# Kernel optimization log

Measured on AMD Instinct MI355X. Metric: run time of the kernel, lower is better.

## Reference

```python
import jax, jax.numpy as jnp
import numpy as np

MAX_SCALE_CAP = 200
STEP = 3


def _shift(a, dy, dx):
    # a[..., y+dy, x+dx] with zero fill outside (dy, dx >= 0), matching the
    # zero-padded dilated 3x3 convs whose only off-center tap is at (+dy,+dx).
    H, W = a.shape[-2], a.shape[-1]
    p = jnp.pad(a, ((0, 0), (0, 0), (0, dy), (0, dx)))
    return p[..., dy:dy + H, dx:dx + W]


def _dif_stacks(Pred, GT, ROI):
    # Builds difPrd / difGT: channel order is (scale major, layer l, direction)
    # directions in dict order: Horizontal (0,+s), Vertical (+s,0), Diagonal (+s,+s)
    B, _, H, W = Pred.shape
    max_scale = min(MAX_SCALE_CAP, max(H, W))
    dP, dG = [], []
    for scale in range(1, max_scale, STEP):
        bP, bG = [], []
        for dy, dx in ((0, scale), (scale, 0), (scale, scale)):
            roi = ROI * _shift(ROI, dy, dx)             # [B,1,H,W]
            bP.append(roi * (Pred - _shift(Pred, dy, dx)))  # [B,3,H,W]
            bG.append(roi * (GT - _shift(GT, dy, dx)))
        # stack dirs on a new axis after layer axis -> l-major, dir-minor
        dP.append(jnp.stack(bP, axis=2).reshape(B, 9, H, W))
        dG.append(jnp.stack(bG, axis=2).reshape(B, 9, H, W))
    return jnp.concatenate(dP, axis=1), jnp.concatenate(dG, axis=1)


def _loss(PredXYZ, GTXYZ, ROIMask):
    difPrd, difGT = _dif_stacks(PredXYZ, GTXYZ, ROIMask)

    # normalization constant per image (detached in the original)
    Rat = jax.nn.relu(difPrd / (difGT + 1e-5))
    absG = jnp.abs(difGT)
    NormConst = (absG * Rat).sum((1, 2, 3)) / ((absG * (Rat > 0)).sum((1, 2, 3)) + 1e-4)
    NormConst = jax.lax.stop_gradient(NormConst)

    c = NormConst                                   # [B]
    safe_c = jnp.where(c > 1e-4, c, 1.0)
    term1 = jnp.where(
        c > 1e-4,
        jnp.abs(difGT - difPrd / safe_c[:, None, None, None]).mean((1, 2, 3)),
        0.0,
    )

    roi_sum = ROIMask.sum((1, 2, 3))
    pos_cnt = (difGT > 0).sum((1, 2, 3)).astype(jnp.float32)
    mean_prd = jnp.abs(difPrd).sum((1, 2, 3)) / pos_cnt

    big = roi_sum > 200
    term2 = jnp.where(big & (mean_prd > 30) & (c > 10), mean_prd - 30.0, 0.0)
    fact = 0.1 / (c + 0.001)
    term3 = jnp.where(big & (mean_prd < 2) & (c < 0.1), (0.2 - mean_prd) * fact, 0.0)

    return (term1 + term2 + term3).sum(), NormConst


def setup_inputs() -> dict:
    key = jax.random.key(0)
    k1, k2, k3 = jax.random.split(key, 3)
    PredXYZ = jax.random.normal(k1, (2, 3, 256, 256), dtype=jnp.float32)
    GTXYZ = jax.random.normal(k2, (2, 3, 256, 256), dtype=jnp.float32)
    ROIMask = (jax.random.uniform(k3, (2, 1, 256, 256)) > 0.3).astype(jnp.float32)
    return {"PredXYZ": PredXYZ, "GTXYZ": GTXYZ, "ROIMask": ROIMask}


def reference(PredXYZ, GTXYZ, ROIMask):
    return _loss(PredXYZ, GTXYZ, ROIMask)
```

## Files before the change

kernel.cpp:

```cpp
#include <hip/hip_runtime.h>


#define NSCALES 67
#define IMG_H 256
#define IMG_W 256
#define NPIX 65536
#define NLINES 2046
#define LMAX_PAD 320


__device__ __forceinline__ double wave_red(double v) {
#pragma unroll
  for (int o = 32; o > 0; o >>= 1) v += __shfl_down(v, o, 64);
  return v;
}

__device__ __forceinline__ void decode_line(int id, int& b, int& base, int& stride, int& L) {
  if (id < 512) {
    b = id >> 8; int y = id & 255;
    base = y * IMG_W; stride = 1; L = IMG_W;
  } else if (id < 1024) {
    int t = id - 512; b = t >> 8;
    base = t & 255; stride = IMG_W; L = IMG_H;
  } else {
    int t = id - 1024; b = (t >= 511) ? 1 : 0;
    int d = t - b * 511; int c = d - 255;
    int ac = (c < 0) ? -c : c;
    base = (c < 0) ? (-c) * IMG_W : c;
    stride = IMG_W + 1; L = 256 - ac;
  }
}

__device__ __forceinline__ int scale_count(int L, int q) {
  int rem = L - 1 - (q << 6);
  int kcnt = (rem >= 1) ? ((rem - 1) / 3 + 1) : 0;
  return (kcnt > NSCALES) ? NSCALES : kcnt;
}

__device__ __forceinline__ float stage_line(
    const float* __restrict__ Pred, const float* __restrict__ GT,
    const float* __restrict__ ROI, int b, int base, int stride, int L,
    int tid, float4* bufA, float4* bufB) {
  const float* P = Pred + b * (3 * NPIX);
  const float* G = GT + b * (3 * NPIX);
  const float* R = ROI + b * NPIX;
  float r = 0.f, p0 = 0.f, p1 = 0.f, p2 = 0.f, g0 = 0.f, g1 = 0.f, g2 = 0.f;
  if (tid < L) {
    int a = base + tid * stride;
    r = R[a];
    p0 = P[a]; p1 = P[a + NPIX]; p2 = P[a + 2 * NPIX];
    g0 = G[a]; g1 = G[a + NPIX]; g2 = G[a + 2 * NPIX];
  }
  bufA[tid] = make_float4(r, p0, p1, p2);
  bufB[tid] = make_float4(g0, g1, g2, 0.f);
  if (tid < LMAX_PAD - 256) {
    bufA[256 + tid] = make_float4(0.f, 0.f, 0.f, 0.f);
    bufB[256 + tid] = make_float4(0.f, 0.f, 0.f, 0.f);
  }
  __syncthreads();
  return r;
}

extern "C" __global__ void __launch_bounds__(256, 8) pass1_kernel(
    const float* __restrict__ Pred, const float* __restrict__ GT,
    const float* __restrict__ ROI, double* __restrict__ ws) {
  __shared__ float4 bufA[LMAX_PAD];
  __shared__ float4 bufB[LMAX_PAD];
  __shared__ double red[4][5];
  const int id = blockIdx.x;
  const int tid = threadIdx.x;
  const int wid = tid >> 6, lane = tid & 63;

  int b, base, stride, L;
  decode_line(id, b, base, stride, L);
  float stg_r = stage_line(Pred, GT, ROI, b, base, stride, L, tid, bufA, bufB);

  float f1 = 0.f, f2 = 0.f, fp = 0.f;
  int pci = 0;
  int P = 0;
  for (int q = 0; q < 4; ++q) {
    const int Kq = scale_count(L, q);
    int k = (wid - P) & 3;
    if (k < Kq) {
      const int c = (q << 6) + lane;
      const float4 cA = bufA[c];
      const float4 cB = bufB[c];
      const float cr = cA.x, cp0 = cA.y, cp1 = cA.z, cp2 = cA.w;
      const float cg0 = cB.x, cg1 = cB.y, cg2 = cB.z;
      const float4* tA = &bufA[c + 1 + 3 * k];
      const float4* tB = &bufB[c + 1 + 3 * k];
#pragma unroll 2
      for (; k < Kq; k += 4) {
        float4 t0 = tA[0];
        float4 t1 = tB[0];
        tA += 12; tB += 12;
        float rr = cr * t0.x;
#define L1BODY(cp, cg, tp, tg)                                   \
        {                                                        \
          float dP = rr * (cp - tp);                             \
          float dG = rr * (cg - tg);                             \
          float qq = dP * __builtin_amdgcn_rcpf(dG + 1e-5f);     \
          float aG = fabsf(dG);                                  \
          f1 += fmaxf(aG * qq, 0.f);                             \
          if (qq > 0.f) f2 += aG;                                \
          if (dG > 0.f) pci++;                                   \
          fp += fabsf(dP);                                       \
        }
        L1BODY(cp0, cg0, t0.y, t1.x)
        L1BODY(cp1, cg1, t0.z, t1.y)
        L1BODY(cp2, cg2, t0.w, t1.z)
#undef L1BODY
      }
    }
    P += Kq;
  }

  double w0 = wave_red((double)f1);
  double w1 = wave_red((double)f2);
  double w2 = wave_red((double)pci);
  double w3 = wave_red((double)fp);
  double w4 = wave_red((double)stg_r);
  if (lane == 0) {
    red[wid][0] = w0; red[wid][1] = w1; red[wid][2] = w2;
    red[wid][3] = w3; red[wid][4] = w4;
  }
  __syncthreads();
  if (tid < 4)
    unsafeAtomicAdd(&ws[b * 4 + tid],
                    red[0][tid] + red[1][tid] + red[2][tid] + red[3][tid]);
  if (tid == 4 && id < 512)
    unsafeAtomicAdd(&ws[8 + b], red[0][4] + red[1][4] + red[2][4] + red[3][4]);
}

extern "C" __global__ void __launch_bounds__(256, 8) pass2_kernel(
    const float* __restrict__ Pred, const float* __restrict__ GT,
    const float* __restrict__ ROI, double* __restrict__ ws) {
  __shared__ float4 bufA[LMAX_PAD];
  __shared__ float4 bufB[LMAX_PAD];
  __shared__ double red[4];
  __shared__ float s_invC;
  const int id = blockIdx.x;
  const int tid = threadIdx.x;
  const int wid = tid >> 6, lane = tid & 63;

  int b, base, stride, L;
  decode_line(id, b, base, stride, L);
  if (tid == 0) {
    double S1 = ws[b * 4 + 0], S2 = ws[b * 4 + 1];
    float cc = (float)(S1 / (S2 + 1e-4));
    s_invC = (cc > 1e-4f) ? (float)(1.0 / (double)cc) : 1.0f;
  }
  stage_line(Pred, GT, ROI, b, base, stride, L, tid, bufA, bufB);

  const float invC = s_invC;
  float f = 0.f;
  int P = 0;
  for (int q = 0; q < 4; ++q) {
    const int Kq = scale_count(L, q);
    int k = (wid - P) & 3;
    if (k < Kq) {
      const int c = (q << 6) + lane;
      const float4 cA = bufA[c];
      const float4 cB = bufB[c];
      const float cr = cA.x, cp0 = cA.y, cp1 = cA.z, cp2 = cA.w;
      const float cg0 = cB.x, cg1 = cB.y, cg2 = cB.z;
      const float4* tA = &bufA[c + 1 + 3 * k];
      const float4* tB = &bufB[c + 1 + 3 * k];
#pragma unroll 2
      for (; k < Kq; k += 4) {
        float4 t0 = tA[0];
        float4 t1 = tB[0];
        tA += 12; tB += 12;
        float rr = cr * t0.x;
        f += rr * fabsf((cg0 - t1.x) - (cp0 - t0.y) * invC);
        f += rr * fabsf((cg1 - t1.y) - (cp1 - t0.z) * invC);
        f += rr * fabsf((cg2 - t1.z) - (cp2 - t0.w) * invC);
      }
    }
    P += Kq;
  }
  double t = wave_red((double)f);
  if (lane == 0) red[wid] = t;
  __syncthreads();
  if (tid == 0)
    unsafeAtomicAdd(&ws[24 + b], red[0] + red[1] + red[2] + red[3]);
}

extern "C" __global__ void __launch_bounds__(64) final_kernel(
    const double* __restrict__ ws, float* __restrict__ out) {
  if (threadIdx.x == 0) {
    double loss = 0.0;
    for (int b = 0; b < 2; ++b) {
      double S1 = ws[b * 4 + 0], S2 = ws[b * 4 + 1];
      double PC = ws[b * 4 + 2], SP = ws[b * 4 + 3];
      double RS = ws[8 + b];
      float cc = (float)(S1 / (S2 + 1e-4));
      out[1 + b] = cc;
      double term1 = (cc > 1e-4f) ? ws[24 + b] / (603.0 * 65536.0) : 0.0;
      float meanPrd = (float)(SP / PC);
      bool big = RS > 200.0;
      float t2 = (big && meanPrd > 30.f && cc > 10.f) ? (meanPrd - 30.f) : 0.f;
      float fact = 0.1f / (cc + 0.001f);
      float t3 = (big && meanPrd < 2.f && cc < 0.1f) ? (0.2f - meanPrd) * fact : 0.f;
      loss += term1 + (double)(t2 + t3);
    }
    out[0] = (float)loss;
  }
}

extern "C" void kernel_launch(void* const* d_in, const int* in_sizes, int n_in,
                              void* d_out, int out_size, void* d_ws, size_t ws_size,
                              hipStream_t stream) {
  (void)in_sizes; (void)n_in; (void)out_size; (void)ws_size;
  const float* Pred = (const float*)d_in[0];
  const float* GT = (const float*)d_in[1];
  const float* ROI = (const float*)d_in[2];
  float* out = (float*)d_out;
  double* ws = (double*)d_ws;

  hipMemsetAsync(d_ws, 0, 32 * sizeof(double), stream);
  hipLaunchKernelGGL(pass1_kernel, dim3(NLINES), dim3(256), 0, stream,
                     Pred, GT, ROI, ws);
  hipLaunchKernelGGL(pass2_kernel, dim3(NLINES), dim3(256), 0, stream,
                     Pred, GT, ROI, ws);
  hipLaunchKernelGGL(final_kernel, dim3(1), dim3(64), 0, stream, ws, out);
}
```

Measured before the change: 128.1 us.

## Replace global atomics with per-block partial slots and drop workspace memset

```diff
diff --git a/kernel.cpp b/kernel.cpp
--- a/kernel.cpp
+++ b/kernel.cpp
@@ -8,6 +8,8 @@
 #define NLINES 2046
 #define LMAX_PAD 320
 
+
+#define SLOT2_BASE 32768
 
 __device__ __forceinline__ double wave_red(double v) {
 #pragma unroll
@@ -125,11 +127,15 @@
     red[wid][3] = w3; red[wid][4] = w4;
   }
   __syncthreads();
-  if (tid < 4)
-    unsafeAtomicAdd(&ws[b * 4 + tid],
-                    red[0][tid] + red[1][tid] + red[2][tid] + red[3][tid]);
-  if (tid == 4 && id < 512)
-    unsafeAtomicAdd(&ws[8 + b], red[0][4] + red[1][4] + red[2][4] + red[3][4]);
+  if (tid < 16) {
+    const int q = tid & 7, tb = tid >> 3;
+    double v = 0.0;
+    if (tb == b && q < 5) {
+      v = red[0][q] + red[1][q] + red[2][q] + red[3][q];
+      if (q == 4 && id >= 512) v = 0.0;
+    }
+    ws[(size_t)id * 16 + tid] = v;
+  }
 }
 
 extern "C" __global__ void __launch_bounds__(256, 8) pass2_kernel(
@@ -138,21 +144,34 @@
   __shared__ float4 bufA[LMAX_PAD];
   __shared__ float4 bufB[LMAX_PAD];
   __shared__ double red[4];
-  __shared__ float s_invC;
+  __shared__ double pre[4][4];
+  __shared__ float s_invC[2];
   const int id = blockIdx.x;
   const int tid = threadIdx.x;
   const int wid = tid >> 6, lane = tid & 63;
 
   int b, base, stride, L;
   decode_line(id, b, base, stride, L);
-  if (tid == 0) {
-    double S1 = ws[b * 4 + 0], S2 = ws[b * 4 + 1];
+
+  double a0 = 0.0, a1 = 0.0, a2 = 0.0, a3 = 0.0;
+  for (int j = tid; j < NLINES; j += 256) {
+    const double* s = ws + (size_t)j * 16;
+    a0 += s[0]; a1 += s[1]; a2 += s[8]; a3 += s[9];
+  }
+  a0 = wave_red(a0); a1 = wave_red(a1); a2 = wave_red(a2); a3 = wave_red(a3);
+  if (lane == 0) {
+    pre[wid][0] = a0; pre[wid][1] = a1; pre[wid][2] = a2; pre[wid][3] = a3;
+  }
+  __syncthreads();
+  if (tid < 2) {
+    double S1 = pre[0][2 * tid] + pre[1][2 * tid] + pre[2][2 * tid] + pre[3][2 * tid];
+    double S2 = pre[0][2 * tid + 1] + pre[1][2 * tid + 1] + pre[2][2 * tid + 1] + pre[3][2 * tid + 1];
     float cc = (float)(S1 / (S2 + 1e-4));
-    s_invC = (cc > 1e-4f) ? (float)(1.0 / (double)cc) : 1.0f;
+    s_invC[tid] = (cc > 1e-4f) ? (float)(1.0 / (double)cc) : 1.0f;
   }
   stage_line(Pred, GT, ROI, b, base, stride, L, tid, bufA, bufB);
 
-  const float invC = s_invC;
+  const float invC = s_invC[b];
   float f = 0.f;
   int P = 0;
   for (int q = 0; q < 4; ++q) {
@@ -182,21 +201,46 @@
   double t = wave_red((double)f);
   if (lane == 0) red[wid] = t;
   __syncthreads();
-  if (tid == 0)
-    unsafeAtomicAdd(&ws[24 + b], red[0] + red[1] + red[2] + red[3]);
-}
-
-extern "C" __global__ void __launch_bounds__(64) final_kernel(
+  if (tid < 2) {
+    double v = (tid == b) ? (red[0] + red[1] + red[2] + red[3]) : 0.0;
+    ws[SLOT2_BASE + (size_t)id * 2 + tid] = v;
+  }
+}
+
+extern "C" __global__ void __launch_bounds__(256) final_kernel(
     const double* __restrict__ ws, float* __restrict__ out) {
-  if (threadIdx.x == 0) {
+  __shared__ double acc[4][12];
+  const int tid = threadIdx.x;
+  const int wid = tid >> 6, lane = tid & 63;
+  double v[12];
+#pragma unroll
+  for (int i = 0; i < 12; ++i) v[i] = 0.0;
+  for (int j = tid; j < NLINES; j += 256) {
+    const double* s = ws + (size_t)j * 16;
+    v[0] += s[0]; v[1] += s[1]; v[2] += s[2]; v[3] += s[3]; v[4] += s[4];
+    v[5] += s[8]; v[6] += s[9]; v[7] += s[10]; v[8] += s[11]; v[9] += s[12];
+    const double* t = ws + SLOT2_BASE + (size_t)j * 2;
+    v[10] += t[0]; v[11] += t[1];
+  }
+#pragma unroll
+  for (int i = 0; i < 12; ++i) {
+    double r = wave_red(v[i]);
+    if (lane == 0) acc[wid][i] = r;
+  }
+  __syncthreads();
+  if (tid == 0) {
     double loss = 0.0;
     for (int b = 0; b < 2; ++b) {
-      double S1 = ws[b * 4 + 0], S2 = ws[b * 4 + 1];
-      double PC = ws[b * 4 + 2], SP = ws[b * 4 + 3];
-      double RS = ws[8 + b];
+      const int o = b * 5;
+      double S1 = acc[0][o] + acc[1][o] + acc[2][o] + acc[3][o];
+      double S2 = acc[0][o + 1] + acc[1][o + 1] + acc[2][o + 1] + acc[3][o + 1];
+      double PC = acc[0][o + 2] + acc[1][o + 2] + acc[2][o + 2] + acc[3][o + 2];
+      double SP = acc[0][o + 3] + acc[1][o + 3] + acc[2][o + 3] + acc[3][o + 3];
+      double RS = acc[0][o + 4] + acc[1][o + 4] + acc[2][o + 4] + acc[3][o + 4];
+      double T1 = acc[0][10 + b] + acc[1][10 + b] + acc[2][10 + b] + acc[3][10 + b];
       float cc = (float)(S1 / (S2 + 1e-4));
       out[1 + b] = cc;
-      double term1 = (cc > 1e-4f) ? ws[24 + b] / (603.0 * 65536.0) : 0.0;
+      double term1 = (cc > 1e-4f) ? T1 / (603.0 * 65536.0) : 0.0;
       float meanPrd = (float)(SP / PC);
       bool big = RS > 200.0;
       float t2 = (big && meanPrd > 30.f && cc > 10.f) ? (meanPrd - 30.f) : 0.f;
@@ -218,10 +262,9 @@
   float* out = (float*)d_out;
   double* ws = (double*)d_ws;
 
-  hipMemsetAsync(d_ws, 0, 32 * sizeof(double), stream);
   hipLaunchKernelGGL(pass1_kernel, dim3(NLINES), dim3(256), 0, stream,
                      Pred, GT, ROI, ws);
   hipLaunchKernelGGL(pass2_kernel, dim3(NLINES), dim3(256), 0, stream,
                      Pred, GT, ROI, ws);
-  hipLaunchKernelGGL(final_kernel, dim3(1), dim3(64), 0, stream, ws, out);
-}
+  hipLaunchKernelGGL(final_kernel, dim3(1), dim3(256), 0, stream, ws, out);
+}
```

Result: faster. 123.8 us (-3.4%).
